# Kernel tuning notes

Hardware: AMD Instinct MI355X
Metric: run time of the kernel (lower is better)

Reference implementation:

```python
import jax, jax.numpy as jnp
import numpy as np
import math

N_NODES = 50000
N_EDGES = 10000
NNZ = 800000
F_IN = 128
NHID = 128
F_OUT = 64
N_LAYERS = 2
ALPHA = 0.1
LAMDA = 0.5


def setup_inputs() -> dict:
    key = jax.random.key(0)
    ks = jax.random.split(key, 8)
    x = jax.random.normal(ks[0], (N_NODES, F_IN), dtype=jnp.float32)
    vertex = jax.random.randint(ks[1], (NNZ,), 0, N_NODES, dtype=jnp.int32)
    edges = jax.random.randint(ks[2], (NNZ,), 0, N_EDGES, dtype=jnp.int32)
    # parameters (Kaiming-ish scaling)
    W0 = jax.random.normal(ks[3], (F_IN, NHID), dtype=jnp.float32) / np.sqrt(F_IN)
    b0 = jnp.zeros((NHID,), dtype=jnp.float32)
    Ws = jax.random.normal(ks[4], (N_LAYERS, NHID, NHID), dtype=jnp.float32) / np.sqrt(NHID)
    Wout = jax.random.normal(ks[5], (NHID, F_OUT), dtype=jnp.float32) / np.sqrt(NHID)
    bout = jnp.zeros((F_OUT,), dtype=jnp.float32)
    return {"x": x, "W0": W0, "b0": b0, "Ws": Ws, "Wout": Wout,
            "bout": bout, "vertex": vertex, "edges": edges}


def _scatter_mean(src, index, num_segments):
    # src: [nnz, d]; index: [nnz] -> out: [num_segments, d]
    s = jax.ops.segment_sum(src, index, num_segments=num_segments)
    cnt = jax.ops.segment_sum(jnp.ones((src.shape[0],), src.dtype), index,
                              num_segments=num_segments)
    return s / jnp.maximum(cnt, 1.0)[:, None]


def _normalize_l2(X):
    # UniGNN normalize_l2: detached row norm, inf->0 scale
    norm = jax.lax.stop_gradient(jnp.linalg.norm(X, axis=-1, keepdims=True))
    scale = jnp.where(norm > 0, 1.0 / jnp.maximum(norm, 1e-30), 0.0)
    return X * scale


def reference(x, W0, b0, Ws, Wout, bout, vertex, edges):
    x = jax.nn.relu(x @ W0 + b0)          # input Linear + ReLU
    x0 = x
    Xe = None
    for i in range(N_LAYERS):
        beta = math.log(LAMDA / (i + 1) + 1.0)
        Xve = x[vertex]                    # [nnz, nhid] vertex->incidence gather
        Xe = _scatter_mean(Xve, edges, N_EDGES)    # [E, nhid]
        Xev = Xe[edges]                    # [nnz, nhid] edge->incidence gather
        Xv = _scatter_mean(Xev, vertex, N_NODES)   # [N, nhid]
        X = _normalize_l2(Xv)
        Xi = (1.0 - ALPHA) * X + ALPHA * x0
        x = (1.0 - beta) * Xi + beta * (Xi @ Ws[i])
        x = jax.nn.relu(x)
    out = x @ Wout + bout
    return (out, Xe)
```

## Files before the change

kernel.cpp:

```cpp
#include <hip/hip_runtime.h>
#include <hip/hip_bf16.h>
#include <math.h>

#define NODES 50000
#define EDGES 10000
#define NNZ   800000
#define FIN   128
#define NHID  128
#define FOUT  64

#define NPART  8
#define NSLICE 128
#define SLICE  (NNZ / NSLICE)
#define CAP    1024
#define EP     (EDGES / NPART)
#define EWORDS (EDGES / 2)
#define VP     (NODES / NPART)
#define VPW    (VP / 2)
#define VSUB   16
#define SLPER  (NSLICE / VSUB)

#define EFILL  (NPART * NSLICE)
#define VFILL  (NPART * VSUB)
#define WCONV_BLOCKS 128
#define GEMM_BLOCKS  ((NODES + 63) / 64)
#define EDGE_BLOCKS  (EDGES * 64 / 256)
#define NF_BLOCKS    (NODES / 16)

#define XL_STRIDE 144

typedef __attribute__((ext_vector_type(8))) short bf16x8;
typedef __attribute__((ext_vector_type(4))) float f32x4;
typedef unsigned short ushort_t;
typedef unsigned int uint_t;

__device__ __forceinline__ ushort_t f2b(float f) {
    __hip_bfloat16 h = __float2bfloat16(f);
    return *reinterpret_cast<ushort_t*>(&h);
}
__device__ __forceinline__ float u2f(unsigned u) {
    union { unsigned u; float f; } c; c.u = u; return c.f;
}
__device__ __forceinline__ float us2f(ushort_t u) { return u2f((unsigned)u << 16); }
__device__ __forceinline__ unsigned pk2(float lo, float hi) {
    return (unsigned)f2b(lo) | ((unsigned)f2b(hi) << 16);
}
#define ACC8(d)                                             \
    do {                                                    \
        a[0] += u2f((d).x << 16); a[1] += u2f((d).x & 0xffff0000u); \
        a[2] += u2f((d).y << 16); a[3] += u2f((d).y & 0xffff0000u); \
        a[4] += u2f((d).z << 16); a[5] += u2f((d).z & 0xffff0000u); \
        a[6] += u2f((d).w << 16); a[7] += u2f((d).w & 0xffff0000u); \
    } while (0)

__global__ __launch_bounds__(256)
void hist_stage_wconv_kernel(const int* __restrict__ vertex, const int* __restrict__ edges,
                             uint_t* __restrict__ cbe,
                             uint_t* __restrict__ stage_e, uint_t* __restrict__ stage_v,
                             int* __restrict__ cnt_se, int* __restrict__ cnt_sv,
                             const float* __restrict__ W0, const float* __restrict__ Ws,
                             const float* __restrict__ Wout,
                             ushort_t* __restrict__ Wt0, ushort_t* __restrict__ WsT,
                             ushort_t* __restrict__ WoutT) {
    __shared__ uint_t eh[EWORDS];
    __shared__ uint_t cse[NPART], csv[NPART];
    const int t = threadIdx.x;
    if (blockIdx.x < NSLICE) {
        const int b = blockIdx.x;
        for (int w = t; w < EWORDS; w += 256) eh[w] = 0;
        if (t < NPART) { cse[t] = 0; csv[t] = 0; }
        __syncthreads();
        const int base = b * SLICE;
        for (int i = base + t; i < base + SLICE; i += 256) {
            const int e = edges[i], v = vertex[i];
            atomicAdd(&eh[e >> 1], 1u << ((e & 1) * 16));
            const int pe = e / EP;
            const uint_t pose = atomicAdd(&cse[pe], 1u);
            stage_e[(size_t)(pe * NSLICE + b) * CAP + pose] = ((uint_t)e << 16) | (uint_t)v;
            const int pv = v / VP;
            const uint_t posv = atomicAdd(&csv[pv], 1u);
            stage_v[(size_t)(pv * NSLICE + b) * CAP + posv] = ((uint_t)v << 16) | (uint_t)e;
        }
        __syncthreads();
        for (int w = t; w < EWORDS; w += 256) cbe[b * EWORDS + w] = eh[w];
        if (t < NPART) {
            cnt_se[t * NSLICE + b] = (int)cse[t];
            cnt_sv[t * NSLICE + b] = (int)csv[t];
        }
    } else {
        const int i = (blockIdx.x - NSLICE) * 256 + t;
        if (i < 128 * 128) { int c = i >> 7, k = i & 127; Wt0[c * 128 + k] = f2b(W0[k * 128 + c]); }
        if (i < 2 * 128 * 128) {
            int l = i >> 14, r = i & 16383, c = r >> 7, k = r & 127;
            WsT[l * 16384 + c * 128 + k] = f2b(Ws[l * 16384 + k * 128 + c]);
        }
        if (i < 64 * 128) { int c = i >> 7, k = i & 127; WoutT[c * 128 + k] = f2b(Wout[k * 64 + c]); }
    }
}

__global__ __launch_bounds__(256)
void vhist_colscane_kernel(const uint_t* __restrict__ stage_v, const int* __restrict__ cnt_sv,
                           uint_t* __restrict__ cbv,
                           uint_t* __restrict__ cbe, int* __restrict__ cnt_e) {
    const int t = threadIdx.x;
    if (blockIdx.x < VFILL) {
        __shared__ uint_t vh[VPW];
        const int p = blockIdx.x & 7, s = blockIdx.x >> 3;
        for (int w = t; w < VPW; w += 256) vh[w] = 0;
        __syncthreads();
        for (int sl = s * SLPER; sl < (s + 1) * SLPER; ++sl) {
            const int n = cnt_sv[p * NSLICE + sl];
            const uint_t* sv = stage_v + (size_t)(p * NSLICE + sl) * CAP;
            for (int j = t; j < n; j += 256) {
                const int vk = (int)(sv[j] >> 16) - p * VP;
                atomicAdd(&vh[vk >> 1], 1u << ((vk & 1) * 16));
            }
        }
        __syncthreads();
        for (int w = t; w < VPW; w += 256)
            cbv[(size_t)(p * VSUB + s) * VPW + w] = vh[w];
    } else {
        const int flat = (blockIdx.x - VFILL) * 256 + t;
        if (flat < EWORDS) {
            uint_t s0 = 0, s1 = 0;
            for (int b = 0; b < NSLICE; ++b) {
                uint_t* q = &cbe[b * EWORDS + flat];
                const uint_t u = *q; *q = s0 | (s1 << 16);
                s0 += u & 0xffffu; s1 += u >> 16;
            }
            cnt_e[2 * flat]     = (int)s0;
            cnt_e[2 * flat + 1] = (int)s1;
        }
    }
}

__global__ __launch_bounds__(256)
void colscanv_kernel(uint_t* __restrict__ cbv, int* __restrict__ cnt_v) {
    const int flat = blockIdx.x * 256 + (int)threadIdx.x;
    if (flat < NPART * VPW) {
        const int p = flat / VPW, w = flat % VPW;
        uint_t s0 = 0, s1 = 0;
        for (int s = 0; s < VSUB; ++s) {
            uint_t* q = &cbv[(size_t)(p * VSUB + s) * VPW + w];
            const uint_t u = *q; *q = s0 | (s1 << 16);
            s0 += u & 0xffffu; s1 += u >> 16;
        }
        cnt_v[p * VP + 2 * w]     = (int)s0;
        cnt_v[p * VP + 2 * w + 1] = (int)s1;
    }
}

__device__ __forceinline__ void scan_impl(const int* __restrict__ cnt, int* __restrict__ rp,
                                          const int n) {
    __shared__ int wsum[16];
    __shared__ int carry_sh;
    const int t = threadIdx.x, lane = t & 63, w = t >> 6;
    if (t == 0) carry_sh = 0;
    __syncthreads();
    for (int base = 0; base < n; base += 8192) {
        const int idx = base + t * 8;
        int v[8];
        if (idx + 8 <= n) {
            const int4 a = *(const int4*)(cnt + idx);
            const int4 b = *(const int4*)(cnt + idx + 4);
            v[0] = a.x; v[1] = a.y; v[2] = a.z; v[3] = a.w;
            v[4] = b.x; v[5] = b.y; v[6] = b.z; v[7] = b.w;
        } else {
#pragma unroll
            for (int j = 0; j < 8; ++j) v[j] = (idx + j < n) ? cnt[idx + j] : 0;
        }
        int sum8 = 0;
#pragma unroll
        for (int j = 0; j < 8; ++j) sum8 += v[j];
        int x = sum8;
#pragma unroll
        for (int o = 1; o < 64; o <<= 1) {
            int y = __shfl_up(x, o);
            if (lane >= o) x += y;
        }
        if (lane == 63) wsum[w] = x;
        __syncthreads();
        if (t < 16) {
            int s = wsum[t];
#pragma unroll
            for (int o = 1; o < 16; o <<= 1) {
                int y = __shfl_up(s, o);
                if (t >= o) s += y;
            }
            wsum[t] = s;
        }
        __syncthreads();
        const int carry = carry_sh;
        int pre = carry + (x - sum8) + (w ? wsum[w - 1] : 0);
        if (idx < n) {
#pragma unroll
            for (int j = 0; j < 8; ++j)
                if (idx + j < n) { rp[idx + j] = pre; pre += v[j]; }
        }
        __syncthreads();
        if (t == 1023) carry_sh = carry + wsum[15];
        __syncthreads();
    }
    if (t == 0) rp[n] = carry_sh;
}

__global__ __launch_bounds__(1024)
void scan2_kernel(const int* __restrict__ cnt_e, int* __restrict__ rp_e,
                  const int* __restrict__ cnt_v, int* __restrict__ rp_v) {
    if (blockIdx.x == 0) scan_impl(cnt_e, rp_e, EDGES);
    else                 scan_impl(cnt_v, rp_v, NODES);
}

__global__ __launch_bounds__(256)
void fill_gemm_kernel(const uint_t* __restrict__ stage_e, const uint_t* __restrict__ stage_v,
                      const int* __restrict__ cnt_se, const int* __restrict__ cnt_sv,
                      const uint_t* __restrict__ cbe, const uint_t* __restrict__ cbv,
                      const int* __restrict__ rp_e, const int* __restrict__ rp_v,
                      ushort_t* __restrict__ col_e, ushort_t* __restrict__ col_v,
                      const float* __restrict__ X, const ushort_t* __restrict__ Wt,
                      const float* __restrict__ bias, ushort_t* __restrict__ x0) {
    __shared__ uint_t cur[VP];
    const int t = threadIdx.x;
    if (blockIdx.x < EFILL) {
        const int p = blockIdx.x & 7, sl = blockIdx.x >> 3;
        for (int k = t; k < EP; k += 256) {
            const int key = p * EP + k;
            const uint_t word = cbe[sl * EWORDS + (key >> 1)];
            const uint_t b16 = (k & 1) ? (word >> 16) : (word & 0xffffu);
            cur[k] = (uint_t)rp_e[key] + b16;
        }
        __syncthreads();
        const int n = cnt_se[p * NSLICE + sl];
        const uint_t* se = stage_e + (size_t)(p * NSLICE + sl) * CAP;
        for (int j = t; j < n; j += 256) {
            const uint_t u = se[j];
            const uint_t pos = atomicAdd(&cur[(int)(u >> 16) - p * EP], 1u);
            col_e[pos] = (ushort_t)(u & 0xffffu);
        }
        return;
    }
    if (blockIdx.x < EFILL + VFILL) {
        const int vb = blockIdx.x - EFILL;
        const int p = vb & 7, s = vb >> 3;
        for (int k = t; k < VP; k += 256) {
            const int key = p * VP + k;
            const uint_t word = cbv[(size_t)(p * VSUB + s) * VPW + (k >> 1)];
            const uint_t b16 = (k & 1) ? (word >> 16) : (word & 0xffffu);
            cur[k] = (uint_t)rp_v[key] + b16;
        }
        __syncthreads();
        for (int sl = s * SLPER; sl < (s + 1) * SLPER; ++sl) {
            const int n = cnt_sv[p * NSLICE + sl];
            const uint_t* sv = stage_v + (size_t)(p * NSLICE + sl) * CAP;
            for (int j = t; j < n; j += 256) {
                const uint_t u = sv[j];
                const uint_t pos = atomicAdd(&cur[(int)(u >> 16) - p * VP], 1u);
                col_v[pos] = (ushort_t)(u & 0xffffu);
            }
        }
        return;
    }
    const int lane = threadIdx.x & 63, wave = threadIdx.x >> 6;
    const int row0 = (blockIdx.x - (EFILL + VFILL)) * 64 + wave * 16;
    if (row0 >= NODES) return;
    const int r = lane & 15, kb = lane >> 4;
    const int row = row0 + r;
    bf16x8 a[4];
#pragma unroll
    for (int k0 = 0; k0 < 4; ++k0) {
        const float* p = X + (size_t)row * FIN + k0 * 32 + kb * 8;
        const float4 lo = *(const float4*)p;
        const float4 hi = *(const float4*)(p + 4);
        bf16x8 tt;
        tt[0] = f2b(lo.x); tt[1] = f2b(lo.y); tt[2] = f2b(lo.z); tt[3] = f2b(lo.w);
        tt[4] = f2b(hi.x); tt[5] = f2b(hi.y); tt[6] = f2b(hi.z); tt[7] = f2b(hi.w);
        a[k0] = tt;
    }
    f32x4 acc[8];
#pragma unroll
    for (int c0 = 0; c0 < 8; ++c0) {
        const float bv = bias[c0 * 16 + r];
        acc[c0] = (f32x4){bv, bv, bv, bv};
    }
#pragma unroll
    for (int k0 = 0; k0 < 4; ++k0)
#pragma unroll
        for (int c0 = 0; c0 < 8; ++c0) {
            const bf16x8 b = *(const bf16x8*)(Wt + (size_t)(c0 * 16 + r) * FIN + k0 * 32 + kb * 8);
            acc[c0] = __builtin_amdgcn_mfma_f32_16x16x32_bf16(a[k0], b, acc[c0], 0, 0, 0);
        }
#pragma unroll
    for (int c0 = 0; c0 < 8; ++c0) {
        const int col = c0 * 16 + r;
#pragma unroll
        for (int v = 0; v < 4; ++v) {
            const int orow = row0 + kb * 4 + v;
            float val = acc[c0][v];
            val = val > 0.f ? val : 0.f;
            x0[(size_t)orow * NHID + col] = f2b(val);
        }
    }
}

__global__ __launch_bounds__(256)
void edge_gather_kernel(const ushort_t* __restrict__ x, const int* __restrict__ rp,
                        const ushort_t* __restrict__ ci, ushort_t* __restrict__ Xe,
                        float* __restrict__ out_xe) {
    const int e = (blockIdx.x * 256 + (int)threadIdx.x) >> 6;
    if (e >= EDGES) return;
    const int lane = threadIdx.x & 63;
    const int sub = lane >> 4, lr = lane & 15;
    const int beg = rp[e], end = rp[e + 1];
    float a[8] = {};
    for (int base = beg; base < end; base += 64) {
        const int m = min(64, end - base);
        const int idx_l = (lane < m) ? (int)ci[base + lane] : 0;
#pragma unroll
        for (int jb = 0; jb < 4; ++jb) {
            uint4 d[4];
#pragma unroll
            for (int j = 0; j < 4; ++j) {
                const int slot = (jb * 4 + j) * 4 + sub;
                const int src = __shfl(idx_l, slot & 63);
                if (slot < m) d[j] = *(const uint4*)(x + (size_t)src * NHID + lr * 8);
            }
#pragma unroll
            for (int j = 0; j < 4; ++j)
                if ((jb * 4 + j) * 4 + sub < m) ACC8(d[j]);
        }
    }
#pragma unroll
    for (int k = 0; k < 8; ++k) {
        a[k] += __shfl_xor(a[k], 16);
        a[k] += __shfl_xor(a[k], 32);
    }
    const float inv = 1.f / (float)max(end - beg, 1);
    if (sub == 0) {
        float vv[8];
#pragma unroll
        for (int k = 0; k < 8; ++k) vv[k] = a[k] * inv;
        uint4 o;
        o.x = pk2(vv[0], vv[1]); o.y = pk2(vv[2], vv[3]);
        o.z = pk2(vv[4], vv[5]); o.w = pk2(vv[6], vv[7]);
        *(uint4*)(Xe + (size_t)e * NHID + lr * 8) = o;
        if (out_xe) {
            const float4 f0 = {vv[0], vv[1], vv[2], vv[3]};
            const float4 f1 = {vv[4], vv[5], vv[6], vv[7]};
            *(float4*)(out_xe + (size_t)e * NHID + lr * 8) = f0;
            *(float4*)(out_xe + (size_t)e * NHID + lr * 8 + 4) = f1;
        }
    }
}

__device__ __forceinline__ void node_phase1(const ushort_t* __restrict__ Xe,
                                            const int* __restrict__ rp,
                                            const ushort_t* __restrict__ ci,
                                            const ushort_t* __restrict__ x0,
                                            const int vbase,
                                            ushort_t* __restrict__ xl) {
    const int lane = threadIdx.x & 63, wave = threadIdx.x >> 6;
    const int sub = lane >> 4, lr = lane & 15;
    const int row = wave * 4 + sub;
    const int v = vbase + row;
    const int beg = rp[v], end = rp[v + 1];
    const int sbase = lane & 48;
    const uint4 u0 = *(const uint4*)(x0 + (size_t)v * NHID + lr * 8);
    float a[8] = {};
    for (int base = beg; base < end; base += 16) {
        const int m = min(16, end - base);
        const int idx_l = (lr < m) ? (int)ci[base + lr] : 0;
#pragma unroll
        for (int jb = 0; jb < 4; ++jb) {
            uint4 d[4];
#pragma unroll
            for (int j = 0; j < 4; ++j) {
                const int slot = jb * 4 + j;
                const int src = __shfl(idx_l, sbase + slot);
                if (slot < m) d[j] = *(const uint4*)(Xe + (size_t)src * NHID + lr * 8);
            }
#pragma unroll
            for (int j = 0; j < 4; ++j)
                if (jb * 4 + j < m) ACC8(d[j]);
        }
    }
    const float inv = 1.f / (float)max(end - beg, 1);
    float mk[8], s = 0.f;
#pragma unroll
    for (int k = 0; k < 8; ++k) { mk[k] = a[k] * inv; s += mk[k] * mk[k]; }
    s += __shfl_xor(s, 1); s += __shfl_xor(s, 2);
    s += __shfl_xor(s, 4); s += __shfl_xor(s, 8);
    const float norm = sqrtf(s);
    const float scale = norm > 0.f ? 1.f / fmaxf(norm, 1e-30f) : 0.f;
    float xv[8];
    xv[0] = u2f(u0.x << 16); xv[1] = u2f(u0.x & 0xffff0000u);
    xv[2] = u2f(u0.y << 16); xv[3] = u2f(u0.y & 0xffff0000u);
    xv[4] = u2f(u0.z << 16); xv[5] = u2f(u0.z & 0xffff0000u);
    xv[6] = u2f(u0.w << 16); xv[7] = u2f(u0.w & 0xffff0000u);
    float o[8];
#pragma unroll
    for (int k = 0; k < 8; ++k) o[k] = 0.9f * mk[k] * scale + 0.1f * xv[k];
    uint4 ou;
    ou.x = pk2(o[0], o[1]); ou.y = pk2(o[2], o[3]);
    ou.z = pk2(o[4], o[5]); ou.w = pk2(o[6], o[7]);
    *(uint4*)(xl + row * XL_STRIDE + lr * 8) = ou;
}

__global__ __launch_bounds__(256)
void node_l1_kernel(const ushort_t* __restrict__ Xe, const int* __restrict__ rp,
                    const ushort_t* __restrict__ ci, const ushort_t* __restrict__ x0,
                    const ushort_t* __restrict__ Wt, float beta,
                    ushort_t* __restrict__ xout) {
    __shared__ ushort_t xl[16 * XL_STRIDE];
    const int vbase = blockIdx.x * 16;
    node_phase1(Xe, rp, ci, x0, vbase, xl);
    __syncthreads();
    const int lane = threadIdx.x & 63, wave = threadIdx.x >> 6;
    const int r = lane & 15, kb = lane >> 4;
    bf16x8 a2[4];
#pragma unroll
    for (int k0 = 0; k0 < 4; ++k0)
        a2[k0] = *(const bf16x8*)(xl + r * XL_STRIDE + k0 * 32 + kb * 8);
    f32x4 acc[2] = {};
#pragma unroll
    for (int k0 = 0; k0 < 4; ++k0)
#pragma unroll
        for (int cc = 0; cc < 2; ++cc) {
            const int c0 = wave * 2 + cc;
            const bf16x8 b = *(const bf16x8*)(Wt + (size_t)(c0 * 16 + r) * NHID + k0 * 32 + kb * 8);
            acc[cc] = __builtin_amdgcn_mfma_f32_16x16x32_bf16(a2[k0], b, acc[cc], 0, 0, 0);
        }
    const float xim = 1.f - beta;
#pragma unroll
    for (int cc = 0; cc < 2; ++cc) {
        const int col = (wave * 2 + cc) * 16 + r;
#pragma unroll
        for (int v = 0; v < 4; ++v) {
            const int row = kb * 4 + v;
            const float xi = us2f(xl[row * XL_STRIDE + col]);
            float val = xim * xi + beta * acc[cc][v];
            val = val > 0.f ? val : 0.f;
            xout[(size_t)(vbase + row) * NHID + col] = f2b(val);
        }
    }
}

__global__ __launch_bounds__(256)
void node_l2_out_kernel(const ushort_t* __restrict__ Xe, const int* __restrict__ rp,
                        const ushort_t* __restrict__ ci, const ushort_t* __restrict__ x0,
                        const ushort_t* __restrict__ Wt, const ushort_t* __restrict__ WoT,
                        const float* __restrict__ bias, float beta,
                        float* __restrict__ out) {
    __shared__ ushort_t xl[16 * XL_STRIDE];
    __shared__ ushort_t x2[16 * XL_STRIDE];
    const int vbase = blockIdx.x * 16;
    node_phase1(Xe, rp, ci, x0, vbase, xl);
    __syncthreads();
    const int lane = threadIdx.x & 63, wave = threadIdx.x >> 6;
    const int r = lane & 15, kb = lane >> 4;
    {
        bf16x8 a2[4];
#pragma unroll
        for (int k0 = 0; k0 < 4; ++k0)
            a2[k0] = *(const bf16x8*)(xl + r * XL_STRIDE + k0 * 32 + kb * 8);
        f32x4 acc[2] = {};
#pragma unroll
        for (int k0 = 0; k0 < 4; ++k0)
#pragma unroll
            for (int cc = 0; cc < 2; ++cc) {
                const int c0 = wave * 2 + cc;
                const bf16x8 b = *(const bf16x8*)(Wt + (size_t)(c0 * 16 + r) * NHID + k0 * 32 + kb * 8);
                acc[cc] = __builtin_amdgcn_mfma_f32_16x16x32_bf16(a2[k0], b, acc[cc], 0, 0, 0);
            }
        const float xim = 1.f - beta;
#pragma unroll
        for (int cc = 0; cc < 2; ++cc) {
            const int col = (wave * 2 + cc) * 16 + r;
#pragma unroll
            for (int v = 0; v < 4; ++v) {
                const int row = kb * 4 + v;
                const float xi = us2f(xl[row * XL_STRIDE + col]);
                float val = xim * xi + beta * acc[cc][v];
                val = val > 0.f ? val : 0.f;
                x2[row * XL_STRIDE + col] = f2b(val);
            }
        }
    }
    __syncthreads();
    bf16x8 a3[4];
#pragma unroll
    for (int k0 = 0; k0 < 4; ++k0)
        a3[k0] = *(const bf16x8*)(x2 + r * XL_STRIDE + k0 * 32 + kb * 8);
    const float bv = bias[wave * 16 + r];
    f32x4 facc = (f32x4){bv, bv, bv, bv};
#pragma unroll
    for (int k0 = 0; k0 < 4; ++k0) {
        const bf16x8 b = *(const bf16x8*)(WoT + (size_t)(wave * 16 + r) * NHID + k0 * 32 + kb * 8);
        facc = __builtin_amdgcn_mfma_f32_16x16x32_bf16(a3[k0], b, facc, 0, 0, 0);
    }
#pragma unroll
    for (int v = 0; v < 4; ++v) {
        const int row = kb * 4 + v;
        out[(size_t)(vbase + row) * FOUT + wave * 16 + r] = facc[v];
    }
}

extern "C" void kernel_launch(void* const* d_in, const int* in_sizes, int n_in,
                              void* d_out, int out_size, void* d_ws, size_t ws_size,
                              hipStream_t stream) {
    const float* x_in  = (const float*)d_in[0];
    const float* W0    = (const float*)d_in[1];
    const float* b0    = (const float*)d_in[2];
    const float* Ws    = (const float*)d_in[3];
    const float* Wout  = (const float*)d_in[4];
    const float* bout  = (const float*)d_in[5];
    const int* vertex  = (const int*)d_in[6];
    const int* edges   = (const int*)d_in[7];

    ushort_t* Xe   = (ushort_t*)d_ws;
    ushort_t* x    = Xe + (size_t)EDGES * NHID;
    ushort_t* x0   = x  + (size_t)NODES * NHID;
    ushort_t* Wt0  = x0 + (size_t)NODES * NHID;
    ushort_t* WsT  = Wt0 + 128 * 128;
    ushort_t* WoutT= WsT + 2 * 128 * 128;
    int* cnt_e = (int*)(WoutT + 64 * 128);
    int* cnt_v = cnt_e + EDGES;
    int* rp_e  = cnt_v + NODES;
    int* rp_v  = rp_e + EDGES + 4;
    int* cnt_se = rp_v + NODES + 4;
    int* cnt_sv = cnt_se + NPART * NSLICE;
    uint_t* cbe = (uint_t*)(cnt_sv + NPART * NSLICE);
    uint_t* cbv = cbe + (size_t)NSLICE * EWORDS;
    uint_t* stage_e = cbv + (size_t)NPART * VSUB * VPW;
    uint_t* stage_v = stage_e + (size_t)NPART * NSLICE * CAP;
    ushort_t* col_e = (ushort_t*)(stage_v + (size_t)NPART * NSLICE * CAP);
    ushort_t* col_v = col_e + NNZ;

    float* out    = (float*)d_out;
    float* out_xe = out + (size_t)NODES * FOUT;

    hist_stage_wconv_kernel<<<NSLICE + WCONV_BLOCKS, 256, 0, stream>>>(
        vertex, edges, cbe, stage_e, stage_v, cnt_se, cnt_sv,
        W0, Ws, Wout, Wt0, WsT, WoutT);
    vhist_colscane_kernel<<<VFILL + (EWORDS + 255) / 256, 256, 0, stream>>>(
        stage_v, cnt_sv, cbv, cbe, cnt_e);
    colscanv_kernel<<<(NPART * VPW + 255) / 256, 256, 0, stream>>>(cbv, cnt_v);
    scan2_kernel<<<2, 1024, 0, stream>>>(cnt_e, rp_e, cnt_v, rp_v);
    fill_gemm_kernel<<<EFILL + VFILL + GEMM_BLOCKS, 256, 0, stream>>>(
        stage_e, stage_v, cnt_se, cnt_sv, cbe, cbv, rp_e, rp_v,
        col_e, col_v, x_in, Wt0, b0, x0);

    const float betas[2] = {logf(1.5f), logf(1.25f)};

    edge_gather_kernel<<<EDGE_BLOCKS, 256, 0, stream>>>(x0, rp_e, col_e, Xe, (float*)nullptr);
    node_l1_kernel<<<NF_BLOCKS, 256, 0, stream>>>(Xe, rp_v, col_v, x0, WsT, betas[0], x);
    edge_gather_kernel<<<EDGE_BLOCKS, 256, 0, stream>>>(x, rp_e, col_e, Xe, out_xe);
    node_l2_out_kernel<<<NF_BLOCKS, 256, 0, stream>>>(
        Xe, rp_v, col_v, x0, WsT + (size_t)NHID * NHID, WoutT, bout, betas[1], out);
}
```

Baseline: 200.6 us.

## Sort nodes by degree to balance per-block work in node kernels

Adds a degree histogram, a bin scan and a counting-sort pass that builds a permutation of nodes grouped by incidence count. The node-layer kernels then process nodes in that order and scatter their results back through a per-block map. Grouping similar-degree nodes into the same 16-node block is meant to cut divergence, where sub-waves idle while waiting on high-degree neighbours. The cost is two extra tiny launches, a memset, atomics, and scattered x0/output row accesses in place of contiguous ones.

```diff
diff --git a/kernel.cpp b/kernel.cpp
--- a/kernel.cpp
+++ b/kernel.cpp
@@ -24,6 +24,8 @@
 #define VFILL  (NPART * VSUB)
 #define WCONV_BLOCKS 128
 #define GEMM_BLOCKS  ((NODES + 63) / 64)
+#define PERMF_BLOCKS 64
+#define NHIST  13
 #define EDGE_BLOCKS  (EDGES * 64 / 256)
 #define NF_BLOCKS    (NODES / 16)
 
@@ -205,10 +207,40 @@
 }
 
 __global__ __launch_bounds__(1024)
-void scan2_kernel(const int* __restrict__ cnt_e, int* __restrict__ rp_e,
-                  const int* __restrict__ cnt_v, int* __restrict__ rp_v) {
-    if (blockIdx.x == 0) scan_impl(cnt_e, rp_e, EDGES);
-    else                 scan_impl(cnt_v, rp_v, NODES);
+void scan2_hist_kernel(const int* __restrict__ cnt_e, int* __restrict__ rp_e,
+                       const int* __restrict__ cnt_v, int* __restrict__ rp_v,
+                       int* __restrict__ dhist) {
+    if (blockIdx.x == 0) { scan_impl(cnt_e, rp_e, EDGES); return; }
+    if (blockIdx.x == 1) { scan_impl(cnt_v, rp_v, NODES); return; }
+    __shared__ int h[256];
+    const int t = threadIdx.x;
+    if (t < 256) h[t] = 0;
+    __syncthreads();
+    for (int v = (blockIdx.x - 2) * 1024 + t; v < NODES; v += NHIST * 1024)
+        atomicAdd(&h[min(cnt_v[v], 255)], 1);
+    __syncthreads();
+    if (t < 256 && h[t]) atomicAdd(&dhist[t], h[t]);
+}
+
+__global__ __launch_bounds__(256)
+void binscan_kernel(const int* __restrict__ dhist, int* __restrict__ bcur) {
+    __shared__ int wsum[4];
+    const int t = threadIdx.x, lane = t & 63, w = t >> 6;
+    const int v = dhist[t];
+    int x = v;
+#pragma unroll
+    for (int o = 1; o < 64; o <<= 1) {
+        int y = __shfl_up(x, o);
+        if (lane >= o) x += y;
+    }
+    if (lane == 63) wsum[w] = x;
+    __syncthreads();
+    if (t == 0) {
+        int s = 0;
+        for (int i = 0; i < 4; ++i) { const int tv = wsum[i]; wsum[i] = s; s += tv; }
+    }
+    __syncthreads();
+    bcur[t] = x - v + wsum[w];
 }
 
 __global__ __launch_bounds__(256)
@@ -218,7 +250,9 @@
                       const int* __restrict__ rp_e, const int* __restrict__ rp_v,
                       ushort_t* __restrict__ col_e, ushort_t* __restrict__ col_v,
                       const float* __restrict__ X, const ushort_t* __restrict__ Wt,
-                      const float* __restrict__ bias, ushort_t* __restrict__ x0) {
+                      const float* __restrict__ bias, ushort_t* __restrict__ x0,
+                      const int* __restrict__ cnt_vd, int* __restrict__ bcur,
+                      int* __restrict__ vperm) {
     __shared__ uint_t cur[VP];
     const int t = threadIdx.x;
     if (blockIdx.x < EFILL) {
@@ -257,6 +291,15 @@
                 const uint_t pos = atomicAdd(&cur[(int)(u >> 16) - p * VP], 1u);
                 col_v[pos] = (ushort_t)(u & 0xffffu);
             }
+        }
+        return;
+    }
+    if (blockIdx.x >= EFILL + VFILL + GEMM_BLOCKS) {
+        const int pb = blockIdx.x - (EFILL + VFILL + GEMM_BLOCKS);
+        for (int v = pb * 256 + t; v < NODES; v += PERMF_BLOCKS * 256) {
+            const int bin = min(cnt_vd[v], 255);
+            const int pos = atomicAdd(&bcur[bin], 1);
+            vperm[pos] = v;
         }
         return;
     }
@@ -356,12 +399,15 @@
                                             const int* __restrict__ rp,
                                             const ushort_t* __restrict__ ci,
                                             const ushort_t* __restrict__ x0,
+                                            const int* __restrict__ vperm,
                                             const int vbase,
-                                            ushort_t* __restrict__ xl) {
+                                            ushort_t* __restrict__ xl,
+                                            int* __restrict__ vmap) {
     const int lane = threadIdx.x & 63, wave = threadIdx.x >> 6;
     const int sub = lane >> 4, lr = lane & 15;
     const int row = wave * 4 + sub;
-    const int v = vbase + row;
+    const int v = vperm[vbase + row];
+    if (lr == 0) vmap[row] = v;
     const int beg = rp[v], end = rp[v + 1];
     const int sbase = lane & 48;
     const uint4 u0 = *(const uint4*)(x0 + (size_t)v * NHID + lr * 8);
@@ -408,11 +454,13 @@
 __global__ __launch_bounds__(256)
 void node_l1_kernel(const ushort_t* __restrict__ Xe, const int* __restrict__ rp,
                     const ushort_t* __restrict__ ci, const ushort_t* __restrict__ x0,
+                    const int* __restrict__ vperm,
                     const ushort_t* __restrict__ Wt, float beta,
                     ushort_t* __restrict__ xout) {
     __shared__ ushort_t xl[16 * XL_STRIDE];
+    __shared__ int vmap[16];
     const int vbase = blockIdx.x * 16;
-    node_phase1(Xe, rp, ci, x0, vbase, xl);
+    node_phase1(Xe, rp, ci, x0, vperm, vbase, xl, vmap);
     __syncthreads();
     const int lane = threadIdx.x & 63, wave = threadIdx.x >> 6;
     const int r = lane & 15, kb = lane >> 4;
@@ -439,7 +487,7 @@
             const float xi = us2f(xl[row * XL_STRIDE + col]);
             float val = xim * xi + beta * acc[cc][v];
             val = val > 0.f ? val : 0.f;
-            xout[(size_t)(vbase + row) * NHID + col] = f2b(val);
+            xout[(size_t)vmap[row] * NHID + col] = f2b(val);
         }
     }
 }
@@ -447,13 +495,15 @@
 __global__ __launch_bounds__(256)
 void node_l2_out_kernel(const ushort_t* __restrict__ Xe, const int* __restrict__ rp,
                         const ushort_t* __restrict__ ci, const ushort_t* __restrict__ x0,
+                        const int* __restrict__ vperm,
                         const ushort_t* __restrict__ Wt, const ushort_t* __restrict__ WoT,
                         const float* __restrict__ bias, float beta,
                         float* __restrict__ out) {
     __shared__ ushort_t xl[16 * XL_STRIDE];
     __shared__ ushort_t x2[16 * XL_STRIDE];
+    __shared__ int vmap[16];
     const int vbase = blockIdx.x * 16;
-    node_phase1(Xe, rp, ci, x0, vbase, xl);
+    node_phase1(Xe, rp, ci, x0, vperm, vbase, xl, vmap);
     __syncthreads();
     const int lane = threadIdx.x & 63, wave = threadIdx.x >> 6;
     const int r = lane & 15, kb = lane >> 4;
@@ -500,7 +550,7 @@
 #pragma unroll
     for (int v = 0; v < 4; ++v) {
         const int row = kb * 4 + v;
-        out[(size_t)(vbase + row) * FOUT + wave * 16 + r] = facc[v];
+        out[(size_t)vmap[row] * FOUT + wave * 16 + r] = facc[v];
     }
 }
 
@@ -528,7 +578,10 @@
     int* rp_v  = rp_e + EDGES + 4;
     int* cnt_se = rp_v + NODES + 4;
     int* cnt_sv = cnt_se + NPART * NSLICE;
-    uint_t* cbe = (uint_t*)(cnt_sv + NPART * NSLICE);
+    int* dhist  = cnt_sv + NPART * NSLICE;
+    int* bcur   = dhist + 256;
+    int* vperm  = bcur + 256;
+    uint_t* cbe = (uint_t*)(vperm + NODES);
     uint_t* cbv = cbe + (size_t)NSLICE * EWORDS;
     uint_t* stage_e = cbv + (size_t)NPART * VSUB * VPW;
     uint_t* stage_v = stage_e + (size_t)NPART * NSLICE * CAP;
@@ -537,6 +590,8 @@
 
     float* out    = (float*)d_out;
     float* out_xe = out + (size_t)NODES * FOUT;
+
+    hipMemsetAsync(dhist, 0, 256 * sizeof(int), stream);
 
     hist_stage_wconv_kernel<<<NSLICE + WCONV_BLOCKS, 256, 0, stream>>>(
         vertex, edges, cbe, stage_e, stage_v, cnt_se, cnt_sv,
@@ -544,16 +599,17 @@
     vhist_colscane_kernel<<<VFILL + (EWORDS + 255) / 256, 256, 0, stream>>>(
         stage_v, cnt_sv, cbv, cbe, cnt_e);
     colscanv_kernel<<<(NPART * VPW + 255) / 256, 256, 0, stream>>>(cbv, cnt_v);
-    scan2_kernel<<<2, 1024, 0, stream>>>(cnt_e, rp_e, cnt_v, rp_v);
-    fill_gemm_kernel<<<EFILL + VFILL + GEMM_BLOCKS, 256, 0, stream>>>(
+    scan2_hist_kernel<<<2 + NHIST, 1024, 0, stream>>>(cnt_e, rp_e, cnt_v, rp_v, dhist);
+    binscan_kernel<<<1, 256, 0, stream>>>(dhist, bcur);
+    fill_gemm_kernel<<<EFILL + VFILL + GEMM_BLOCKS + PERMF_BLOCKS, 256, 0, stream>>>(
         stage_e, stage_v, cnt_se, cnt_sv, cbe, cbv, rp_e, rp_v,
-        col_e, col_v, x_in, Wt0, b0, x0);
+        col_e, col_v, x_in, Wt0, b0, x0, cnt_v, bcur, vperm);
 
     const float betas[2] = {logf(1.5f), logf(1.25f)};
 
     edge_gather_kernel<<<EDGE_BLOCKS, 256, 0, stream>>>(x0, rp_e, col_e, Xe, (float*)nullptr);
-    node_l1_kernel<<<NF_BLOCKS, 256, 0, stream>>>(Xe, rp_v, col_v, x0, WsT, betas[0], x);
+    node_l1_kernel<<<NF_BLOCKS, 256, 0, stream>>>(Xe, rp_v, col_v, x0, vperm, WsT, betas[0], x);
     edge_gather_kernel<<<EDGE_BLOCKS, 256, 0, stream>>>(x, rp_e, col_e, Xe, out_xe);
     node_l2_out_kernel<<<NF_BLOCKS, 256, 0, stream>>>(
-        Xe, rp_v, col_v, x0, WsT + (size_t)NHID * NHID, WoutT, bout, betas[1], out);
-}
+        Xe, rp_v, col_v, x0, vperm, WsT + (size_t)NHID * NHID, WoutT, bout, betas[1], out);
+}
```

After: 342.2 us. +70.6%, slower.
